# Optimization experiments

Measured on AMD Instinct MI355X. Metric: run time of the kernel, lower is better.

## Reference

```python
import jax, jax.numpy as jnp
import numpy as np

RADIUS = 0.4
SIGMA = 0.08
DIM_OUT = 64


def setup_inputs() -> dict:
    key = jax.random.key(0)
    k1, k2, k3, k4 = jax.random.split(key, 4)
    m, b, nc, ks, na = 1024, 2, 64, 13, 20
    frag = jax.random.uniform(k1, (m, 3), dtype=jnp.float32)          # (m,3) raw points in unit cube
    clouds = jax.random.uniform(k2, (b, 3, nc), dtype=jnp.float32)    # (b,3,nc) == n_center -> no FPS
    # anchor-rotated kernel points, |p| <= 0.7*radius (KERNEL_CONDENSE_RATIO)
    kernels = (jax.random.uniform(k3, (ks, na, 3), dtype=jnp.float32) - 0.5) * (2.0 * 0.7 * RADIUS)
    # BasicSO3Conv weight, xavier_normal with relu gain on (dim_out, 1, ks): std = sqrt(2)*sqrt(2/(ks + dim_out*ks))
    std = np.sqrt(2.0) * np.sqrt(2.0 / (ks + DIM_OUT * ks))
    W = jax.random.normal(k4, (DIM_OUT, ks), dtype=jnp.float32) * std
    return {"frag": frag, "clouds": clouds, "kernels": kernels, "W": W}


def reference(frag, clouds, kernels, W):
    # frag (m,3), clouds (b,3,nc), kernels (ks,na,3), W (dim_out, ks)
    centers = clouds                                   # clouds.shape[2] == n_center -> skip FPS
    c = jnp.transpose(centers, (0, 2, 1))              # (b,nc,3)
    b, nc, _ = c.shape
    ks, na, _ = kernels.shape

    # ball query: points within radius of each center
    d2c = jnp.sum((frag[None, :, None, :] - c[:, None, :, :]) ** 2, axis=-1)   # (b,m,nc)
    mask = (d2c < RADIUS * RADIUS).astype(frag.dtype)                          # (b,m,nc)
    nnctn = jnp.sum(mask, axis=1)                                              # (b,nc)

    # gaussian weight of each in-ball point w.r.t. each rotated kernel point location
    kpos = c[:, :, None, None, :] + kernels[None, None, :, :, :]               # (b,nc,ks,na,3)
    fn2 = jnp.sum(frag * frag, axis=-1)                                        # (m,)
    pn2 = jnp.sum(kpos * kpos, axis=-1)                                        # (b,nc,ks,na)
    dot = jnp.einsum('md,bnkad->bmnka', frag, kpos)                            # (b,m,nc,ks,na)
    d2k = fn2[None, :, None, None, None] + pn2[:, None] - 2.0 * dot            # (b,m,nc,ks,na)
    w = jnp.exp(-d2k / (2.0 * SIGMA)) * mask[:, :, :, None, None]

    wts = jnp.transpose(jnp.sum(w, axis=1), (0, 2, 1, 3))                      # (b,ks,nc,na)
    wts = wts / (nnctn[:, None, :, None] + 1.0)

    # BasicSO3Conv: view (b, dim_in*ks, nc*na), W @ x, view back (dim_in=1)
    x = wts.reshape(b, ks, nc * na)
    feats = jnp.einsum('ok,bkp->bop', W, x).reshape(b, W.shape[0], nc, na)     # (b,dim_out,nc,na)
    return feats
```

## Files before the change

kernel.cpp:

```cpp
#include <hip/hip_runtime.h>
#include <hip/hip_bf16.h>

#define M_PTS   1024
#define B_SZ    2
#define NC      64
#define KS      13
#define NA      20
#define DIM_OUT 64

#define NBLK_PER_C 5
#define A_SLICE    4
#define NITEMS     (KS * A_SLICE)

static constexpr float R2    = 0.4f * 0.4f;
static constexpr float C2SIG = 6.25f * 1.44269504088896340736f;

__global__ __launch_bounds__(64)
void KernelPropagation_24206435681031_kernel(const float* __restrict__ frag,
                                             const float* __restrict__ clouds,
                                             const float* __restrict__ kernels,
                                             const float* __restrict__ W,
                                             float* __restrict__ out)
{
    const int g  = blockIdx.x;
    const int bc = g / NBLK_PER_C;
    const int sl = g % NBLK_PER_C;
    const int b  = bc / NC;
    const int n  = bc % NC;
    const int t  = threadIdx.x;

    __shared__ float4 pf[M_PTS];
    __shared__ float  accs[NITEMS];

    const float cx = clouds[(b * 3 + 0) * NC + n];
    const float cy = clouds[(b * 3 + 1) * NC + n];
    const float cz = clouds[(b * 3 + 2) * NC + n];

    float kx2 = 0.f, ky2 = 0.f, kz2 = 0.f, ek = 0.f;
    if (t < NITEMS) {
        const int k = t >> 2;
        const int a = sl * A_SLICE + (t & 3);
        const int ki = (k * NA + a) * 3;
        const float kx = cx + kernels[ki + 0];
        const float ky = cy + kernels[ki + 1];
        const float kz = cz + kernels[ki + 2];
        const float pn2 = kx * kx + ky * ky + kz * kz;
        ek  = exp2f(-C2SIG * pn2);
        kx2 = (2.0f * C2SIG) * kx;
        ky2 = (2.0f * C2SIG) * ky;
        kz2 = (2.0f * C2SIG) * kz;
    }

    int wbase = 0;
    for (int base = 0; base < M_PTS; base += 64) {
        const int i = base + t;
        const float x = frag[i * 3 + 0];
        const float y = frag[i * 3 + 1];
        const float z = frag[i * 3 + 2];
        const float dx = x - cx, dy = y - cy, dz = z - cz;
        const bool in = (dx * dx + dy * dy + dz * dz) < R2;
        const unsigned long long mask = __ballot(in);
        const int pre = __popcll(mask & ((1ull << t) - 1ull));
        if (in)
            pf[wbase + pre] = make_float4(x, y, z, -C2SIG * (x * x + y * y + z * z));
        wbase += __popcll(mask);
    }
    __syncthreads();

    const int   npts = wbase;
    const float inv  = 1.0f / ((float)npts + 1.0f);

    float s0 = 0.f, s1 = 0.f;
    int j = 0;
    for (; j + 3 < npts; j += 4) {
        const float4 p0 = pf[j + 0];
        const float4 p1 = pf[j + 1];
        const float4 p2 = pf[j + 2];
        const float4 p3 = pf[j + 3];
        float t0 = fmaf(p0.z, kz2, fmaf(p0.y, ky2, p0.x * kx2)) + p0.w;
        float t1 = fmaf(p1.z, kz2, fmaf(p1.y, ky2, p1.x * kx2)) + p1.w;
        float t2 = fmaf(p2.z, kz2, fmaf(p2.y, ky2, p2.x * kx2)) + p2.w;
        float t3 = fmaf(p3.z, kz2, fmaf(p3.y, ky2, p3.x * kx2)) + p3.w;
        s0 = fmaf(ek, exp2f(t0), s0);
        s1 = fmaf(ek, exp2f(t1), s1);
        s0 = fmaf(ek, exp2f(t2), s0);
        s1 = fmaf(ek, exp2f(t3), s1);
    }
    for (; j < npts; ++j) {
        const float4 p0 = pf[j];
        float t0 = fmaf(p0.z, kz2, fmaf(p0.y, ky2, p0.x * kx2)) + p0.w;
        s0 = fmaf(ek, exp2f(t0), s0);
    }
    if (t < NITEMS) accs[t] = (s0 + s1) * inv;
    __syncthreads();

    float f0 = 0.f, f1 = 0.f, f2 = 0.f, f3 = 0.f;
#pragma unroll
    for (int k = 0; k < KS; ++k) {
        const float w = W[t * KS + k];
        f0 = fmaf(w, accs[k * 4 + 0], f0);
        f1 = fmaf(w, accs[k * 4 + 1], f1);
        f2 = fmaf(w, accs[k * 4 + 2], f2);
        f3 = fmaf(w, accs[k * 4 + 3], f3);
    }
    float4* dst = (float4*)(out + ((size_t)(b * DIM_OUT + t) * NC + n) * NA + sl * A_SLICE);
    *dst = make_float4(f0, f1, f2, f3);
}

extern "C" void kernel_launch(void* const* d_in, const int* in_sizes, int n_in,
                              void* d_out, int out_size, void* d_ws, size_t ws_size,
                              hipStream_t stream) {
    const float* frag    = (const float*)d_in[0];
    const float* clouds  = (const float*)d_in[1];
    const float* kernels = (const float*)d_in[2];
    const float* W       = (const float*)d_in[3];
    float* out = (float*)d_out;

    (void)in_sizes; (void)n_in; (void)out_size; (void)d_ws; (void)ws_size;

    KernelPropagation_24206435681031_kernel<<<B_SZ * NC * NBLK_PER_C, 64, 0, stream>>>(
        frag, clouds, kernels, W, out);
}
```

Baseline: 74.71 us.

## Split point loop across four waves per block with shared-memory reduction

Each block now runs four waves instead of one. Ball-query compaction uses a shared atomic counter per wave-ballot, and the gaussian accumulation over in-ball points is split across the waves. Partial sums are then reduced in shared memory, and the output projection is spread across all 256 threads. This is meant to cut the serial per-block latency of the long point loop, since only 640 single-wave blocks ran before. In exchange it adds extra barriers and atomics, and point order becomes nondeterministic, which changes float summation order.

```diff
diff --git a/kernel.cpp b/kernel.cpp
--- a/kernel.cpp
+++ b/kernel.cpp
@@ -11,68 +11,84 @@
 #define NBLK_PER_C 5
 #define A_SLICE    4
 #define NITEMS     (KS * A_SLICE)
+#define NWAVES     4
+#define NTHREADS   (NWAVES * 64)
 
 static constexpr float R2    = 0.4f * 0.4f;
 static constexpr float C2SIG = 6.25f * 1.44269504088896340736f;
 
-__global__ __launch_bounds__(64)
+__global__ __launch_bounds__(NTHREADS)
 void KernelPropagation_24206435681031_kernel(const float* __restrict__ frag,
                                              const float* __restrict__ clouds,
                                              const float* __restrict__ kernels,
                                              const float* __restrict__ W,
                                              float* __restrict__ out)
 {
-    const int g  = blockIdx.x;
-    const int bc = g / NBLK_PER_C;
-    const int sl = g % NBLK_PER_C;
-    const int b  = bc / NC;
-    const int n  = bc % NC;
-    const int t  = threadIdx.x;
+    const int g    = blockIdx.x;
+    const int bc   = g / NBLK_PER_C;
+    const int sl   = g % NBLK_PER_C;
+    const int b    = bc / NC;
+    const int n    = bc % NC;
+    const int t    = threadIdx.x;
+    const int lane = t & 63;
+    const int w    = t >> 6;
 
     __shared__ float4 pf[M_PTS];
+    __shared__ float  part[NWAVES * NITEMS];
     __shared__ float  accs[NITEMS];
+    __shared__ int    cnt;
 
     const float cx = clouds[(b * 3 + 0) * NC + n];
     const float cy = clouds[(b * 3 + 1) * NC + n];
     const float cz = clouds[(b * 3 + 2) * NC + n];
 
-    float kx2 = 0.f, ky2 = 0.f, kz2 = 0.f, ek = 0.f;
-    if (t < NITEMS) {
-        const int k = t >> 2;
-        const int a = sl * A_SLICE + (t & 3);
-        const int ki = (k * NA + a) * 3;
-        const float kx = cx + kernels[ki + 0];
-        const float ky = cy + kernels[ki + 1];
-        const float kz = cz + kernels[ki + 2];
-        const float pn2 = kx * kx + ky * ky + kz * kz;
-        ek  = exp2f(-C2SIG * pn2);
-        kx2 = (2.0f * C2SIG) * kx;
-        ky2 = (2.0f * C2SIG) * ky;
-        kz2 = (2.0f * C2SIG) * kz;
-    }
+    if (t == 0) cnt = 0;
+    __syncthreads();
 
-    int wbase = 0;
-    for (int base = 0; base < M_PTS; base += 64) {
-        const int i = base + t;
+#pragma unroll
+    for (int c4 = 0; c4 < 4; ++c4) {
+        const int i = (w + 4 * c4) * 64 + lane;
         const float x = frag[i * 3 + 0];
         const float y = frag[i * 3 + 1];
         const float z = frag[i * 3 + 2];
         const float dx = x - cx, dy = y - cy, dz = z - cz;
         const bool in = (dx * dx + dy * dy + dz * dz) < R2;
         const unsigned long long mask = __ballot(in);
-        const int pre = __popcll(mask & ((1ull << t) - 1ull));
+        const int tot = __popcll(mask);
+        const int pre = __popcll(mask & ((1ull << lane) - 1ull));
+        int base = 0;
+        if (lane == 0 && tot) base = atomicAdd(&cnt, tot);
+        base = __shfl(base, 0, 64);
         if (in)
-            pf[wbase + pre] = make_float4(x, y, z, -C2SIG * (x * x + y * y + z * z));
-        wbase += __popcll(mask);
+            pf[base + pre] = make_float4(x, y, z, -C2SIG * (x * x + y * y + z * z));
     }
     __syncthreads();
 
-    const int   npts = wbase;
+    const int   npts = cnt;
     const float inv  = 1.0f / ((float)npts + 1.0f);
 
+    const int  item   = lane;
+    const bool active = item < NITEMS;
+    float kx2 = 0.f, ky2 = 0.f, kz2 = 0.f, ek = 0.f;
+    if (active) {
+        const int k  = item >> 2;
+        const int a  = sl * A_SLICE + (item & 3);
+        const int ki = (k * NA + a) * 3;
+        const float kx = cx + kernels[ki + 0];
+        const float ky = cy + kernels[ki + 1];
+        const float kz = cz + kernels[ki + 2];
+        ek  = exp2f(-C2SIG * (kx * kx + ky * ky + kz * kz));
+        kx2 = (2.0f * C2SIG) * kx;
+        ky2 = (2.0f * C2SIG) * ky;
+        kz2 = (2.0f * C2SIG) * kz;
+    }
+
+    const int jlo = (npts * w)     >> 2;
+    const int jhi = (npts * (w+1)) >> 2;
+
     float s0 = 0.f, s1 = 0.f;
-    int j = 0;
-    for (; j + 3 < npts; j += 4) {
+    int j = jlo;
+    for (; j + 3 < jhi; j += 4) {
         const float4 p0 = pf[j + 0];
         const float4 p1 = pf[j + 1];
         const float4 p2 = pf[j + 2];
@@ -86,25 +102,29 @@
         s0 = fmaf(ek, exp2f(t2), s0);
         s1 = fmaf(ek, exp2f(t3), s1);
     }
-    for (; j < npts; ++j) {
+    for (; j < jhi; ++j) {
         const float4 p0 = pf[j];
         float t0 = fmaf(p0.z, kz2, fmaf(p0.y, ky2, p0.x * kx2)) + p0.w;
         s0 = fmaf(ek, exp2f(t0), s0);
     }
-    if (t < NITEMS) accs[t] = (s0 + s1) * inv;
+    if (active) part[w * NITEMS + item] = s0 + s1;
     __syncthreads();
 
-    float f0 = 0.f, f1 = 0.f, f2 = 0.f, f3 = 0.f;
+    if (t < NITEMS) {
+        const float s = part[t] + part[NITEMS + t] + part[2 * NITEMS + t] + part[3 * NITEMS + t];
+        accs[t] = s * inv;
+    }
+    __syncthreads();
+
+    {
+        const int o  = t >> 2;
+        const int jj = t & 3;
+        float f = 0.f;
 #pragma unroll
-    for (int k = 0; k < KS; ++k) {
-        const float w = W[t * KS + k];
-        f0 = fmaf(w, accs[k * 4 + 0], f0);
-        f1 = fmaf(w, accs[k * 4 + 1], f1);
-        f2 = fmaf(w, accs[k * 4 + 2], f2);
-        f3 = fmaf(w, accs[k * 4 + 3], f3);
+        for (int k = 0; k < KS; ++k)
+            f = fmaf(W[o * KS + k], accs[k * 4 + jj], f);
+        out[((size_t)(b * DIM_OUT + o) * NC + n) * NA + sl * A_SLICE + jj] = f;
     }
-    float4* dst = (float4*)(out + ((size_t)(b * DIM_OUT + t) * NC + n) * NA + sl * A_SLICE);
-    *dst = make_float4(f0, f1, f2, f3);
 }
 
 extern "C" void kernel_launch(void* const* d_in, const int* in_sizes, int n_in,
@@ -118,6 +138,6 @@
 
     (void)in_sizes; (void)n_in; (void)out_size; (void)d_ws; (void)ws_size;
 
-    KernelPropagation_24206435681031_kernel<<<B_SZ * NC * NBLK_PER_C, 64, 0, stream>>>(
+    KernelPropagation_24206435681031_kernel<<<B_SZ * NC * NBLK_PER_C, NTHREADS, 0, stream>>>(
         frag, clouds, kernels, W, out);
 }
```

New measurement: 64.65 us. 1.16x faster.
